# Performance work log

Hardware: AMD Instinct MI355X
Metric: run time of the kernel (lower is better)

## Reference

```python
import jax, jax.numpy as jnp
import numpy as np


def setup_inputs() -> dict:
    key = jax.random.key(0)
    ks = jax.random.split(key, 9)
    N, L, E, H = 8, 4096, 1024, 16
    D = E // H
    return {
        "values": jax.random.normal(ks[0], (N, L, E), dtype=jnp.float32),
        "keys": jax.random.normal(ks[1], (N, L, E), dtype=jnp.float32),
        "query": jax.random.normal(ks[2], (N, L, E), dtype=jnp.float32),
        "mask": jax.random.randint(ks[3], (1, 1, H, H), 0, 2, dtype=jnp.int32),
        "Wv": jax.random.normal(ks[4], (D, D), dtype=jnp.float32) / np.sqrt(D),
        "Wk": jax.random.normal(ks[5], (D, D), dtype=jnp.float32) / np.sqrt(D),
        "Wq": jax.random.normal(ks[6], (D, D), dtype=jnp.float32) / np.sqrt(D),
        "Wo": jax.random.normal(ks[7], (E, E), dtype=jnp.float32) / np.sqrt(E),
        "bo": jnp.zeros((E,), dtype=jnp.float32),
    }


def reference(values, keys, query, mask, Wv, Wk, Wq, Wo, bo):
    N, L, E = query.shape
    H = mask.shape[-1]          # heads
    D = E // H                  # head_dim
    # reshape to (N, L, H, D) then per-head Dense(head_dim) on last dim
    v = values.reshape(N, L, H, D) @ Wv
    k = keys.reshape(N, L, H, D) @ Wk
    q = query.reshape(N, L, H, D) @ Wq
    # Faithful to the source: keys transposed with perm [0,1,3,2], so matmul
    # batches over (N, L) and energy is a (H x H) matrix per position.
    energy = jnp.einsum("nlhd,nlgd->nlhg", q, k)  # (N, L, H, H)
    energy = jnp.where(mask == 0, jnp.float32(-1e20), energy)
    attention = jax.nn.softmax(energy / (E ** 0.5), axis=-1)
    out = jnp.einsum("nlhg,nlgd->nlhd", attention, v)  # (N, L, H, D)
    # source: transpose to (N, H, L, D) then reshape to (N, L, H*D)
    out = out.transpose(0, 2, 1, 3).reshape(N, L, H * D)
    out = out @ Wo + bo
    return out, attention
```

## Files before the change

kernel.cpp:

```cpp
#include <hip/hip_runtime.h>

typedef short short8 __attribute__((ext_vector_type(8)));
typedef short short4v __attribute__((ext_vector_type(4)));
typedef float f32x4 __attribute__((ext_vector_type(4)));
typedef unsigned short u16;

#define MFMA16(a, b, c) __builtin_amdgcn_mfma_f32_16x16x32_bf16(a, b, c, 0, 0, 0)
#define GLD_LDS(g, l)                                                          \
  __builtin_amdgcn_global_load_lds(                                            \
      (__attribute__((address_space(1))) void*)(void*)(g),                     \
      (__attribute__((address_space(3))) void*)(l), 16, 0, 0)

__device__ __forceinline__ u16 f2bf(float f) {
  union { float f; unsigned u; } x; x.f = f;
  unsigned r = x.u + 0x7fffu + ((x.u >> 16) & 1u);
  return (u16)(r >> 16);
}

__device__ __forceinline__ short4v pack4(f32x4 a) {
  short4v r;
  r[0] = (short)f2bf(a[0]); r[1] = (short)f2bf(a[1]);
  r[2] = (short)f2bf(a[2]); r[3] = (short)f2bf(a[3]);
  return r;
}

__global__ __launch_bounds__(256) void prep(const float* __restrict__ Wv,
                                            const float* __restrict__ Wk,
                                            const float* __restrict__ Wq,
                                            const float* __restrict__ Wo,
                                            u16* __restrict__ WoT2,
                                            u16* __restrict__ Mt) {
  __shared__ __align__(16) float A[64][65];
  __shared__ __align__(16) float B[64][68];
  const int t = threadIdx.x;
  const int r = t >> 2, c = (t & 3) * 16;
  if (blockIdx.x < 256) {
    const int tr = blockIdx.x >> 4, tc = blockIdx.x & 15;
#pragma unroll
    for (int u = 0; u < 4; ++u)
      *(float4*)&A[r][c + u * 4] = *(const float4*)(Wv + r * 64 + c + u * 4);
#pragma unroll
    for (int u = 0; u < 4; ++u)
      *(float4*)&B[r][c + u * 4] =
          *(const float4*)(Wo + (tr * 64 + r) * 1024 + tc * 64 + c + u * 4);
    __syncthreads();
    const int n = t & 63, i0 = (t >> 6) * 16;
    float acc[16];
#pragma unroll
    for (int ii = 0; ii < 16; ++ii) acc[ii] = 0.f;
    for (int j = 0; j < 64; ++j) {
      const float wo = B[j][n];
#pragma unroll
      for (int ii = 0; ii < 16; ++ii) acc[ii] += A[i0 + ii][j] * wo;
    }
    u16* dst = WoT2 + (size_t)(tc * 64 + n) * 1024 + tr * 64 + i0;
    short8 o0, o1;
#pragma unroll
    for (int jj = 0; jj < 8; ++jj) { o0[jj] = (short)f2bf(acc[jj]); o1[jj] = (short)f2bf(acc[8 + jj]); }
    *(short8*)(void*)dst = o0;
    *(short8*)(void*)(dst + 8) = o1;
  } else {
#pragma unroll
    for (int u = 0; u < 4; ++u)
      *(float4*)&A[r][c + u * 4] = *(const float4*)(Wq + r * 64 + c + u * 4);
#pragma unroll
    for (int u = 0; u < 4; ++u)
      *(float4*)&B[r][c + u * 4] = *(const float4*)(Wk + r * 64 + c + u * 4);
    __syncthreads();
    const int n = t & 63, k0 = (t >> 6) * 16;
    float acc[16];
#pragma unroll
    for (int ii = 0; ii < 16; ++ii) acc[ii] = 0.f;
    for (int d = 0; d < 64; ++d) {
      const float wk = B[n][d];
#pragma unroll
      for (int kk = 0; kk < 16; ++kk) acc[kk] += A[k0 + kk][d] * wk;
    }
    u16* dst = Mt + n * 64 + k0;
    short8 o0, o1;
#pragma unroll
    for (int jj = 0; jj < 8; ++jj) { o0[jj] = (short)f2bf(acc[jj]); o1[jj] = (short)f2bf(acc[8 + jj]); }
    *(short8*)(void*)dst = o0;
    *(short8*)(void*)(dst + 8) = o1;
  }
}

__global__ __launch_bounds__(256, 4) void attn_kernel(
    const float* __restrict__ values, const float* __restrict__ keys,
    const float* __restrict__ query, const int* __restrict__ mask,
    const u16* __restrict__ Mt, float* __restrict__ attn,
    u16* __restrict__ out2) {
  __shared__ __align__(16) u16 x1[4][16][68];
  __shared__ __align__(16) u16 x2[4][16][68];
  __shared__ __align__(16) u16 vT[4][64][24];
  __shared__ __align__(16) u16 mt_lds[64][68];
  __shared__ int mask_lds[256];

  const int tid = threadIdx.x;
  const int w = tid >> 6, lane = tid & 63;
  const int g16 = lane & 15;
  const int q4 = lane >> 4;
  const int kbase = q4 * 8;
  const int mrow = q4 * 4;

  {
    const short8* mg = (const short8*)Mt;
    short8 a0 = mg[tid];
    short8 a1 = mg[256 + tid];
    *(short8*)&mt_lds[tid >> 3][(tid & 7) * 8] = a0;
    const int g1 = 256 + tid;
    *(short8*)&mt_lds[g1 >> 3][(g1 & 7) * 8] = a1;
    mask_lds[tid] = mask[tid];
  }
  __syncthreads();

  int mzb = 0;
#pragma unroll
  for (int r = 0; r < 4; ++r)
    mzb |= (mask_lds[(mrow + r) * 16 + g16] == 0) ? (1 << r) : 0;

  const f32x4 zero = {0.f, 0.f, 0.f, 0.f};
  const int pbase = blockIdx.x * 16 + w * 4;

  const f32x4* qv = (const f32x4*)query;
  const f32x4* kv = (const f32x4*)keys;
  const f32x4* vv = (const f32x4*)values;
  const size_t b0 = (size_t)pbase * 256 + lane;

  f32x4 qf0 = qv[b0], qf1 = qv[b0 + 64], qf2 = qv[b0 + 128], qf3 = qv[b0 + 192];
  f32x4 kf0 = kv[b0], kf1 = kv[b0 + 64], kf2 = kv[b0 + 128], kf3 = kv[b0 + 192];
  f32x4 vf0 = vv[b0], vf1 = vv[b0 + 64], vf2 = vv[b0 + 128], vf3 = vv[b0 + 192];

  const int wr = lane >> 4;
  const int wc = (lane & 15) * 4;

#pragma unroll
  for (int i = 0; i < 4; ++i) {
    const int p = pbase + i;

    *(short4v*)&x1[w][0 + wr][wc] = pack4(qf0);
    *(short4v*)&x1[w][4 + wr][wc] = pack4(qf1);
    *(short4v*)&x1[w][8 + wr][wc] = pack4(qf2);
    *(short4v*)&x1[w][12 + wr][wc] = pack4(qf3);
    *(short4v*)&x2[w][0 + wr][wc] = pack4(kf0);
    *(short4v*)&x2[w][4 + wr][wc] = pack4(kf1);
    *(short4v*)&x2[w][8 + wr][wc] = pack4(kf2);
    *(short4v*)&x2[w][12 + wr][wc] = pack4(kf3);
#pragma unroll
    for (int j = 0; j < 4; ++j) {
      vT[w][wc + j][0 + wr] = f2bf(vf0[j]);
      vT[w][wc + j][4 + wr] = f2bf(vf1[j]);
      vT[w][wc + j][8 + wr] = f2bf(vf2[j]);
      vT[w][wc + j][12 + wr] = f2bf(vf3[j]);
    }

    if (i < 3) {
      const size_t nb = b0 + (size_t)(i + 1) * 256;
      qf0 = qv[nb]; qf1 = qv[nb + 64]; qf2 = qv[nb + 128]; qf3 = qv[nb + 192];
      kf0 = kv[nb]; kf1 = kv[nb + 64]; kf2 = kv[nb + 128]; kf3 = kv[nb + 192];
      vf0 = vv[nb]; vf1 = vv[nb + 64]; vf2 = vv[nb + 128]; vf3 = vv[nb + 192];
    }

    short8 aq0 = *(const short8*)&x1[w][g16][kbase];
    short8 aq1 = *(const short8*)&x1[w][g16][32 + kbase];
    short8 ak0 = *(const short8*)&x2[w][g16][kbase];
    short8 ak1 = *(const short8*)&x2[w][g16][32 + kbase];
    short8 mtf[2][4];
#pragma unroll
    for (int kb = 0; kb < 2; ++kb)
#pragma unroll
      for (int nc = 0; nc < 4; ++nc)
        mtf[kb][nc] = *(const short8*)&mt_lds[nc * 16 + g16][kb * 32 + kbase];

    f32x4 tacc[4];
#pragma unroll
    for (int nc = 0; nc < 4; ++nc) {
      tacc[nc] = MFMA16(aq0, mtf[0][nc], zero);
      tacc[nc] = MFMA16(aq1, mtf[1][nc], tacc[nc]);
    }
#pragma unroll
    for (int nc = 0; nc < 4; ++nc)
#pragma unroll
      for (int r = 0; r < 4; ++r)
        x1[w][mrow + r][nc * 16 + g16] = f2bf(tacc[nc][r]);

    short8 ea0 = *(const short8*)&x1[w][g16][kbase];
    short8 ea1 = *(const short8*)&x1[w][g16][32 + kbase];
    f32x4 acce = MFMA16(ea0, ak0, zero);
    acce = MFMA16(ea1, ak1, acce);

    const float SC = 0.045084220027780106f;
    float* x1f = (float*)&x1[w][0][0];
#pragma unroll
    for (int r = 0; r < 4; ++r) {
      const float val = ((mzb >> r) & 1) ? -45.f : acce[r] * SC;
      const float pe = exp2f(val);
      float s = pe;
      s += __shfl_xor(s, 1, 16);
      s += __shfl_xor(s, 2, 16);
      s += __shfl_xor(s, 4, 16);
      s += __shfl_xor(s, 8, 16);
      const float a = pe * __builtin_amdgcn_rcpf(s);
      x1f[(mrow + r) * 34 + g16] = a;
      x2[w][mrow + r][g16] = f2bf(a);
    }

    {
      f32x4 av = *(const f32x4*)&x1f[(lane >> 2) * 34 + (lane & 3) * 4];
      *(f32x4*)(attn + (size_t)p * 256 + lane * 4) = av;
    }

    short8 pa;
    if (lane < 32) {
      pa = *(const short8*)&x2[w][g16][kbase];
    } else {
      short8 z = {0, 0, 0, 0, 0, 0, 0, 0};
      pa = z;
    }
    const int gsel = (lane < 32) ? kbase : 0;
#pragma unroll
    for (int nc = 0; nc < 4; ++nc) {
      short8 vb = *(const short8*)&vT[w][nc * 16 + g16][gsel];
      f32x4 acco = MFMA16(pa, vb, zero);
#pragma unroll
      for (int r = 0; r < 4; ++r)
        x1[w][mrow + r][nc * 16 + g16] = f2bf(acco[r]);
    }

    {
      short8 s0 = *(const short8*)&x1[w][lane >> 3][(lane & 7) * 8];
      short8 s1 = *(const short8*)&x1[w][8 + (lane >> 3)][(lane & 7) * 8];
      u16* dst = out2 + (size_t)p * 1024 + lane * 8;
      *(short8*)(void*)dst = s0;
      *(short8*)(void*)(dst + 512) = s1;
    }
  }
}

__global__ __launch_bounds__(256, 2) void gemm_kernel(
    const u16* __restrict__ A, const u16* __restrict__ BT,
    const float* __restrict__ bo, float* __restrict__ C) {
  __shared__ __align__(16) u16 As[128 * 32];
  __shared__ __align__(16) u16 Bs[128 * 32];
  const int t = threadIdx.x, lane = t & 63;
  const int g16 = lane & 15, q4 = lane >> 4;
  const int w = t >> 6, wm = w >> 1, wn = w & 1;
  const int bm = blockIdx.x & 255, bn = blockIdx.x >> 8;

  f32x4 acc[4][4];
  const f32x4 zero = {0.f, 0.f, 0.f, 0.f};
#pragma unroll
  for (int mt = 0; mt < 4; ++mt)
#pragma unroll
    for (int nt = 0; nt < 4; ++nt) acc[mt][nt] = zero;

  const int am = t >> 2, ak = (t & 3) * 8;
  const int R0 = bm * 128 + am;
  const int R1 = R0 + 64;
  const size_t base0 =
      ((size_t)((R0 >> 12) * 4096 + (R0 & 255) * 16)) * 1024 +
      ((R0 & 4095) >> 8) * 64;
  const size_t base1 =
      ((size_t)((R1 >> 12) * 4096 + (R1 & 255) * 16)) * 1024 +
      ((R1 & 4095) >> 8) * 64;
  const u16* ga0 = A + base0 + ak;
  const u16* ga1 = A + base1 + ak;
  const u16* gb = BT + (size_t)(bn * 128 + am) * 1024 + ak;
  u16* lA = &As[t * 8];
  u16* lB = &Bs[t * 8];

  for (int kt = 0; kt < 32; ++kt) {
    __syncthreads();
    const int aoff = (kt >> 1) * 1024 + (kt & 1) * 32;
    const int ko = kt * 32;
    GLD_LDS(ga0 + aoff, lA);
    GLD_LDS(ga1 + aoff, lA + 2048);
    GLD_LDS(gb + ko, lB);
    GLD_LDS(gb + 64 * 1024 + ko, lB + 2048);
    __syncthreads();

    short8 af[4], bf[4];
#pragma unroll
    for (int mt = 0; mt < 4; ++mt)
      af[mt] = *(const short8*)&As[(wm * 64 + mt * 16 + g16) * 32 + q4 * 8];
#pragma unroll
    for (int nt = 0; nt < 4; ++nt)
      bf[nt] = *(const short8*)&Bs[(wn * 64 + nt * 16 + g16) * 32 + q4 * 8];
#pragma unroll
    for (int mt = 0; mt < 4; ++mt)
#pragma unroll
      for (int nt = 0; nt < 4; ++nt)
        acc[mt][nt] = MFMA16(af[mt], bf[nt], acc[mt][nt]);
  }

#pragma unroll
  for (int nt = 0; nt < 4; ++nt) {
    const int col = bn * 128 + wn * 64 + nt * 16 + g16;
    const float bias = bo[col];
#pragma unroll
    for (int mt = 0; mt < 4; ++mt) {
#pragma unroll
      for (int r = 0; r < 4; ++r) {
        const int row = bm * 128 + wm * 64 + mt * 16 + q4 * 4 + r;
        C[(size_t)row * 1024 + col] = acc[mt][nt][r] + bias;
      }
    }
  }
}

extern "C" void kernel_launch(void* const* d_in, const int* in_sizes, int n_in,
                              void* d_out, int out_size, void* d_ws,
                              size_t ws_size, hipStream_t stream) {
  const float* values = (const float*)d_in[0];
  const float* keys   = (const float*)d_in[1];
  const float* query  = (const float*)d_in[2];
  const int*   mask   = (const int*)d_in[3];
  const float* Wv = (const float*)d_in[4];
  const float* Wk = (const float*)d_in[5];
  const float* Wq = (const float*)d_in[6];
  const float* Wo = (const float*)d_in[7];
  const float* bo = (const float*)d_in[8];

  float* out  = (float*)d_out;
  float* attn = out + 33554432;

  u16* out2 = (u16*)d_ws;
  u16* WoT2 = out2 + 33554432;
  u16* Mt   = WoT2 + 1048576;

  prep<<<257, 256, 0, stream>>>(Wv, Wk, Wq, Wo, WoT2, Mt);
  attn_kernel<<<2048, 256, 0, stream>>>(values, keys, query, mask, Mt, attn,
                                        out2);
  gemm_kernel<<<2048, 256, 0, stream>>>(out2, WoT2, bo, out);
}
```

Measured before the change: 234.6 us.

## Hoist Mt fragments to registers, pack bf16 stores, permute V layout, direct attn stores

Loads the Mt weight fragments into registers once before the loop, reusing x1 as temporary staging so the mt_lds and mask_lds buffers disappear. Mask is now read from global memory. bf16 conversions are packed two per 32-bit word, so V is written with 8-byte stores in a permuted column order, and the attention probabilities use a matching permuted index. Attention probabilities go straight to global memory with scalar stores instead of through an LDS transpose. The aim is to cut LDS traffic and footprint to raise occupancy, at the cost of more registers and less coalesced attn writes.

```diff
diff --git a/kernel.cpp b/kernel.cpp
--- a/kernel.cpp
+++ b/kernel.cpp
@@ -1,7 +1,7 @@
 #include <hip/hip_runtime.h>
 
 typedef short short8 __attribute__((ext_vector_type(8)));
-typedef short short4v __attribute__((ext_vector_type(4)));
+typedef unsigned uint2v __attribute__((ext_vector_type(2)));
 typedef float f32x4 __attribute__((ext_vector_type(4)));
 typedef unsigned short u16;
 
@@ -17,10 +17,13 @@
   return (u16)(r >> 16);
 }
 
-__device__ __forceinline__ short4v pack4(f32x4 a) {
-  short4v r;
-  r[0] = (short)f2bf(a[0]); r[1] = (short)f2bf(a[1]);
-  r[2] = (short)f2bf(a[2]); r[3] = (short)f2bf(a[3]);
+__device__ __forceinline__ unsigned pk2(float a, float b) {
+  return (unsigned)f2bf(a) | ((unsigned)f2bf(b) << 16);
+}
+__device__ __forceinline__ uint2v pk4(f32x4 a) {
+  uint2v r;
+  r[0] = pk2(a[0], a[1]);
+  r[1] = pk2(a[2], a[3]);
   return r;
 }
 
@@ -92,9 +95,7 @@
     u16* __restrict__ out2) {
   __shared__ __align__(16) u16 x1[4][16][68];
   __shared__ __align__(16) u16 x2[4][16][68];
-  __shared__ __align__(16) u16 vT[4][64][24];
-  __shared__ __align__(16) u16 mt_lds[64][68];
-  __shared__ int mask_lds[256];
+  __shared__ __align__(16) u16 vTp[4][64][24];
 
   const int tid = threadIdx.x;
   const int w = tid >> 6, lane = tid & 63;
@@ -102,22 +103,30 @@
   const int q4 = lane >> 4;
   const int kbase = q4 * 8;
   const int mrow = q4 * 4;
-
+  const int pg16 = (g16 & 3) * 4 + (g16 >> 2);
+
+  u16 (*mt)[68] = (u16(*)[68]) & x1[0][0][0];
   {
     const short8* mg = (const short8*)Mt;
     short8 a0 = mg[tid];
     short8 a1 = mg[256 + tid];
-    *(short8*)&mt_lds[tid >> 3][(tid & 7) * 8] = a0;
+    *(short8*)&mt[tid >> 3][(tid & 7) * 8] = a0;
     const int g1 = 256 + tid;
-    *(short8*)&mt_lds[g1 >> 3][(g1 & 7) * 8] = a1;
-    mask_lds[tid] = mask[tid];
+    *(short8*)&mt[g1 >> 3][(g1 & 7) * 8] = a1;
   }
   __syncthreads();
+  short8 mtf[2][4];
+#pragma unroll
+  for (int kb = 0; kb < 2; ++kb)
+#pragma unroll
+    for (int nc = 0; nc < 4; ++nc)
+      mtf[kb][nc] = *(const short8*)&mt[nc * 16 + g16][kb * 32 + kbase];
+  __syncthreads();
 
   int mzb = 0;
 #pragma unroll
   for (int r = 0; r < 4; ++r)
-    mzb |= (mask_lds[(mrow + r) * 16 + g16] == 0) ? (1 << r) : 0;
+    mzb |= (mask[(mrow + r) * 16 + g16] == 0) ? (1 << r) : 0;
 
   const f32x4 zero = {0.f, 0.f, 0.f, 0.f};
   const int pbase = blockIdx.x * 16 + w * 4;
@@ -138,20 +147,20 @@
   for (int i = 0; i < 4; ++i) {
     const int p = pbase + i;
 
-    *(short4v*)&x1[w][0 + wr][wc] = pack4(qf0);
-    *(short4v*)&x1[w][4 + wr][wc] = pack4(qf1);
-    *(short4v*)&x1[w][8 + wr][wc] = pack4(qf2);
-    *(short4v*)&x1[w][12 + wr][wc] = pack4(qf3);
-    *(short4v*)&x2[w][0 + wr][wc] = pack4(kf0);
-    *(short4v*)&x2[w][4 + wr][wc] = pack4(kf1);
-    *(short4v*)&x2[w][8 + wr][wc] = pack4(kf2);
-    *(short4v*)&x2[w][12 + wr][wc] = pack4(kf3);
+    *(uint2v*)&x1[w][0 + wr][wc] = pk4(qf0);
+    *(uint2v*)&x1[w][4 + wr][wc] = pk4(qf1);
+    *(uint2v*)&x1[w][8 + wr][wc] = pk4(qf2);
+    *(uint2v*)&x1[w][12 + wr][wc] = pk4(qf3);
+    *(uint2v*)&x2[w][0 + wr][wc] = pk4(kf0);
+    *(uint2v*)&x2[w][4 + wr][wc] = pk4(kf1);
+    *(uint2v*)&x2[w][8 + wr][wc] = pk4(kf2);
+    *(uint2v*)&x2[w][12 + wr][wc] = pk4(kf3);
 #pragma unroll
     for (int j = 0; j < 4; ++j) {
-      vT[w][wc + j][0 + wr] = f2bf(vf0[j]);
-      vT[w][wc + j][4 + wr] = f2bf(vf1[j]);
-      vT[w][wc + j][8 + wr] = f2bf(vf2[j]);
-      vT[w][wc + j][12 + wr] = f2bf(vf3[j]);
+      uint2v col;
+      col[0] = pk2(vf0[j], vf1[j]);
+      col[1] = pk2(vf2[j], vf3[j]);
+      *(uint2v*)&vTp[w][wc + j][wr * 4] = col;
     }
 
     if (i < 3) {
@@ -160,17 +169,12 @@
       kf0 = kv[nb]; kf1 = kv[nb + 64]; kf2 = kv[nb + 128]; kf3 = kv[nb + 192];
       vf0 = vv[nb]; vf1 = vv[nb + 64]; vf2 = vv[nb + 128]; vf3 = vv[nb + 192];
     }
+    __builtin_amdgcn_sched_barrier(0);
 
     short8 aq0 = *(const short8*)&x1[w][g16][kbase];
     short8 aq1 = *(const short8*)&x1[w][g16][32 + kbase];
     short8 ak0 = *(const short8*)&x2[w][g16][kbase];
     short8 ak1 = *(const short8*)&x2[w][g16][32 + kbase];
-    short8 mtf[2][4];
-#pragma unroll
-    for (int kb = 0; kb < 2; ++kb)
-#pragma unroll
-      for (int nc = 0; nc < 4; ++nc)
-        mtf[kb][nc] = *(const short8*)&mt_lds[nc * 16 + g16][kb * 32 + kbase];
 
     f32x4 tacc[4];
 #pragma unroll
@@ -190,7 +194,7 @@
     acce = MFMA16(ea1, ak1, acce);
 
     const float SC = 0.045084220027780106f;
-    float* x1f = (float*)&x1[w][0][0];
+    float* ap = attn + (size_t)p * 256 + mrow * 16 + g16;
 #pragma unroll
     for (int r = 0; r < 4; ++r) {
       const float val = ((mzb >> r) & 1) ? -45.f : acce[r] * SC;
@@ -201,13 +205,8 @@
       s += __shfl_xor(s, 4, 16);
       s += __shfl_xor(s, 8, 16);
       const float a = pe * __builtin_amdgcn_rcpf(s);
-      x1f[(mrow + r) * 34 + g16] = a;
-      x2[w][mrow + r][g16] = f2bf(a);
-    }
-
-    {
-      f32x4 av = *(const f32x4*)&x1f[(lane >> 2) * 34 + (lane & 3) * 4];
-      *(f32x4*)(attn + (size_t)p * 256 + lane * 4) = av;
+      ap[r * 16] = a;
+      x2[w][mrow + r][pg16] = f2bf(a);
     }
 
     short8 pa;
@@ -220,7 +219,7 @@
     const int gsel = (lane < 32) ? kbase : 0;
 #pragma unroll
     for (int nc = 0; nc < 4; ++nc) {
-      short8 vb = *(const short8*)&vT[w][nc * 16 + g16][gsel];
+      short8 vb = *(const short8*)&vTp[w][nc * 16 + g16][gsel];
       f32x4 acco = MFMA16(pa, vb, zero);
 #pragma unroll
       for (int r = 0; r < 4; ++r)
```

Result: no change. 236.8 us (+1.0%).
